# Optimization experiments

Measured on AMD Instinct MI355X. Metric: run time of the kernel, lower is better.

The kernel has to match this reference:

```python
import jax, jax.numpy as jnp
import numpy as np

WIN = 9  # window_size (isotropic, module default)
EPS = 1e-5


def _box_sum3d(x, win):
    """Sum over a win^3 box, same-size output ('same' padding). x: [B,1,D,H,W].
    The ones kernel is separable, so apply three 1D convolutions."""
    pad = win // 2
    for ax in range(3):  # spatial axes D,H,W
        kshape = [1, 1, 1, 1, 1]
        kshape[2 + ax] = win
        k = jnp.ones(kshape, x.dtype)
        padding = [(0, 0)] * 3
        padding[ax] = (pad, pad)
        x = jax.lax.conv_general_dilated(x, k, window_strides=(1, 1, 1), padding=padding)
    return x


def setup_inputs() -> dict:
    key = jax.random.key(0)
    k1, k2 = jax.random.split(key)
    shape = (2, 1, 160, 192, 160)
    y_pred = jax.random.normal(k1, shape, dtype=jnp.float32)
    y_true = jax.random.normal(k2, shape, dtype=jnp.float32)
    return {"y_pred": y_pred, "y_true": y_true}


def reference(y_pred, y_true):
    I, J = y_true, y_pred
    win_size = jnp.asarray(WIN ** 3, I.dtype)  # 729

    I_sum = _box_sum3d(I, WIN)
    J_sum = _box_sum3d(J, WIN)
    I2_sum = _box_sum3d(I * I, WIN)
    J2_sum = _box_sum3d(J * J, WIN)
    IJ_sum = _box_sum3d(I * J, WIN)

    I_mean = I_sum / win_size
    J_mean = J_sum / win_size

    cross = IJ_sum - J_mean * I_sum - I_mean * J_sum + I_mean * J_mean * win_size
    I_var = I2_sum - 2 * I_mean * I_sum + I_mean * I_mean * win_size
    J_var = J2_sum - 2 * J_mean * J_sum + J_mean * J_mean * win_size

    cc = cross * cross / (I_var * J_var + EPS)
    return -jnp.mean(cc)
```

## Files before the change

kernel.cpp:

```cpp
#include <hip/hip_runtime.h>
#include <hip/hip_fp16.h>


#define B_    2
#define D_    160
#define H_    192
#define W_    160
#define HW_   (H_*W_)

#define RS    12
#define SLS   (24*RS)
#define FS    (2*SLS)
#define RAWSZ (5*FS)
#define ZROW  (2*RAWSZ)
#define ZEND  (ZROW + 16)
#define HSUM0 ZEND
#define HCS   160
#define HRS   10
#define HSZ   (10*HCS)
#define REDU  (HSUM0 + 2*HSZ)
#define SMEM  (REDU + 8)
#define DC    80
#define ZCH   (D_/DC)
#define NMAC  ((DC+8)/2)
#define W3I   (1.0f/729.0f)
#define NTOT  9830400.0f

#if __has_builtin(__builtin_amdgcn_rcpf)
#define RCP(x) __builtin_amdgcn_rcpf(x)
#else
#define RCP(x) (1.0f/(x))
#endif

typedef _Float16 half8 __attribute__((ext_vector_type(8)));
typedef float    f32x4 __attribute__((ext_vector_type(4)));
typedef unsigned u32x2 __attribute__((ext_vector_type(2)));
#define MFMA16(a,b,c) __builtin_amdgcn_mfma_f32_16x16x32_f16((a),(b),(c),0,0,0)

#if __has_builtin(__builtin_amdgcn_permlane32_swap)
#define PL32(a,b) do { u32x2 _s = __builtin_amdgcn_permlane32_swap((a),(b),false,false); \
                       (a)=_s[0]; (b)=_s[1]; } while(0)
#else
#define PL32(a,b) asm volatile("s_nop 1\nv_permlane32_swap_b32 %0, %1" : "+v"(a), "+v"(b))
#endif
#if __has_builtin(__builtin_amdgcn_permlane16_swap)
#define PL16(a,b) do { u32x2 _s = __builtin_amdgcn_permlane16_swap((a),(b),false,false); \
                       (a)=_s[0]; (b)=_s[1]; } while(0)
#else
#define PL16(a,b) asm volatile("s_nop 1\nv_permlane16_swap_b32 %0, %1" : "+v"(a), "+v"(b))
#endif

struct __align__(8) HP { __half2 a, b; };

__global__ __launch_bounds__(256, 4) void ncc_fused(const float* __restrict__ gI,
                                                    const float* __restrict__ gJ,
                                                    float* __restrict__ out)
{
  __shared__ __align__(16) float sm[SMEM];
  const int tid  = threadIdx.x;
  const int lane = tid & 63;
  const int Q    = tid >> 6;
  const int n15  = lane & 15;
  const int q4   = lane >> 4;
  const int w0   = blockIdx.x * 16;
  const int h0   = blockIdx.y * 16;
  const int bz   = blockIdx.z;
  const int bb   = bz / ZCH;
  const int d_lo = (bz % ZCH) * DC;

  for (int i = tid; i < ZEND; i += 256) sm[i] = 0.f;

  half8 SEL;
  #pragma unroll
  for (int j = 0; j < 8; ++j) {
    const int k = 8*q4 + j;
    SEL[j] = (k >= n15 && k <= n15 + 8) ? (_Float16)1 : (_Float16)0;
  }

  bool val0 = false, val1 = false;
  int  lo0 = 0, lo1 = 0, sc0 = 0, sc1 = 0;
  const float *pi0 = gI, *pj0 = gJ, *pi1 = gI, *pj1 = gJ;
  {
    auto prep = [&](int t, bool& val, int& lo, int& sc,
                    const float*& pi, const float*& pj) {
      if (t >= 288) { val = false; return; }
      sc = t / 144;
      const int u = t - sc*144;
      const int r = u / 6, c = u - r*6;
      const int gh = h0 - 4 + r, gw = w0 - 4 + 4*c;
      val = ((unsigned)gh < (unsigned)H_) && (gw >= 0) && (gw + 3 < W_);
      lo  = sc*SLS + r*RS + 2*c;
      const long off = ((long)(bb*D_ + (d_lo - 4 + sc))*H_ + gh)*(long)W_ + gw;
      pi = gI + off; pj = gJ + off;
    };
    prep(tid, val0, lo0, sc0, pi0, pj0);
    prep((tid >= 224) ? tid + 32 : 512, val1, lo1, sc1, pi1, pj1);
  }

  int rb_[3], hb_[3];
  #pragma unroll
  for (int i = 0; i < 3; ++i) {
    int c = Q + 4*i; if (c > 9) c = 9;
    rb_[i] = (c % 5)*FS + (c / 5)*SLS;
    hb_[i] = HSUM0 + c*HCS;
  }
  const int a1r = n15*RS + 4*q4;
  const int a2r = (n15 < 8) ? ((16 + n15)*RS + 4*q4) : -1;
  const int zr  = ZROW + 4*q4;

  const int rh = tid >> 4, rw = tid & 15;
  const int rbase = HSUM0 + rw*HRS + (rh >> 1);
  const int rsh   = (rh & 1) * 16;

  float ring[5][9], S[5];
  #pragma unroll
  for (int f = 0; f < 5; ++f) {
    S[f] = 0.f;
    #pragma unroll
    for (int k = 0; k < 9; ++k) ring[f][k] = 0.f;
  }
  float acc = 0.f;

  float4 f0i = {0,0,0,0}, f0j = {0,0,0,0}, f1i = {0,0,0,0}, f1j = {0,0,0,0};
  auto fetch = [&](int sbase) {
    if (val0 && (unsigned)(sbase + sc0) < (unsigned)D_) {
      f0i = *(const float4*)pi0; f0j = *(const float4*)pj0;
    } else { f0i = make_float4(0,0,0,0); f0j = make_float4(0,0,0,0); }
    pi0 += 2*HW_; pj0 += 2*HW_;
    if (val1 && (unsigned)(sbase + sc1) < (unsigned)D_) {
      f1i = *(const float4*)pi1; f1j = *(const float4*)pj1;
    } else { f1i = make_float4(0,0,0,0); f1j = make_float4(0,0,0,0); }
    pi1 += 2*HW_; pj1 += 2*HW_;
  };

  auto stage_one = [&](int lo, float4 fi, float4 fj) {
    const __half2 i01 = __floats2half2_rn(fi.x, fi.y);
    const __half2 i23 = __floats2half2_rn(fi.z, fi.w);
    const __half2 j01 = __floats2half2_rn(fj.x, fj.y);
    const __half2 j23 = __floats2half2_rn(fj.z, fj.w);
    HP hI; hI.a = i01; hI.b = i23;
    HP hJ; hJ.a = j01; hJ.b = j23;
    HP h2; h2.a = __hmul2(i01, i01); h2.b = __hmul2(i23, i23);
    HP h3; h3.a = __hmul2(j01, j01); h3.b = __hmul2(j23, j23);
    HP h4; h4.a = __hmul2(i01, j01); h4.b = __hmul2(i23, j23);
    *(HP*)&sm[lo]        = hI;
    *(HP*)&sm[lo +   FS] = hJ;
    *(HP*)&sm[lo + 2*FS] = h2;
    *(HP*)&sm[lo + 3*FS] = h3;
    *(HP*)&sm[lo + 4*FS] = h4;
  };
  auto stage_write = [&](int buf) {
    const int b = buf * RAWSZ;
    if (val0) stage_one(b + lo0, f0i, f0j);
    if (val1) stage_one(b + lo1, f1i, f1j);
  };

  auto chain = [&](int rb, int hb) {
    const half8 A1 = *(const half8*)&sm[rb + a1r];
    const half8 A2 = (a2r >= 0) ? *(const half8*)&sm[rb + a2r]
                                : *(const half8*)&sm[zr];
    const f32x4 z = {0.f, 0.f, 0.f, 0.f};
    const f32x4 d1 = MFMA16(A1, SEL, z);
    const f32x4 d2 = MFMA16(A2, SEL, z);
    unsigned t0 = __builtin_bit_cast(unsigned, __floats2half2_rn(d1[0], d1[1]));
    unsigned t1 = __builtin_bit_cast(unsigned, __floats2half2_rn(d1[2], d1[3]));
    unsigned u0 = __builtin_bit_cast(unsigned, __floats2half2_rn(d2[0], d2[1]));
    unsigned u1 = __builtin_bit_cast(unsigned, __floats2half2_rn(d2[2], d2[3]));
    PL32(t0, u0);
    PL32(t1, u1);
    PL16(t0, u0);
    PL16(t1, u1);
    union { unsigned u[4]; half8 h; } Bv;
    Bv.u[0] = t0; Bv.u[1] = t1; Bv.u[2] = u0; Bv.u[3] = u1;
    const f32x4 dh = MFMA16(SEL, Bv.h, z);
    HP ph; ph.a = __floats2half2_rn(dh[0], dh[1]); ph.b = __floats2half2_rn(dh[2], dh[3]);
    *(HP*)&sm[hb + n15*HRS + 2*q4] = ph;
  };

  auto h2ext = [&](int addr) -> float {
    const unsigned u = *(const unsigned*)&sm[addr];
    return __half2float(__ushort_as_half((unsigned short)(u >> rsh)));
  };
  auto ring_cc = [&](int m, int hB) {
    float nA[5], nB[5];
    #pragma unroll
    for (int f = 0; f < 5; ++f) {
      nA[f] = h2ext(rbase + hB + f*HCS);
      nB[f] = h2ext(rbase + hB + (5 + f)*HCS);
    }
    float SA[5], SB[5];
    #pragma unroll
    for (int f = 0; f < 5; ++f) {
      SA[f] = S[f]  + nA[f] - ring[f][8];
      SB[f] = SA[f] + nB[f] - ring[f][7];
      S[f]  = SB[f];
      #pragma unroll
      for (int k = 8; k >= 2; --k) ring[f][k] = ring[f][k-2];
      ring[f][1] = nA[f]; ring[f][0] = nB[f];
    }
    if (m >= 4) {
      {
        const float cr = SA[4] - SA[0]*SA[1]*W3I;
        const float vi = SA[2] - SA[0]*SA[0]*W3I;
        const float vj = SA[3] - SA[1]*SA[1]*W3I;
        acc += cr*cr * RCP(vi*vj + 1e-5f);
      }
      {
        const float cr = SB[4] - SB[0]*SB[1]*W3I;
        const float vi = SB[2] - SB[0]*SB[0]*W3I;
        const float vj = SB[3] - SB[1]*SB[1]*W3I;
        acc += cr*cr * RCP(vi*vj + 1e-5f);
      }
    }
  };

  fetch(d_lo - 4);
  __syncthreads();
  stage_write(0);
  fetch(d_lo - 2);
  __syncthreads();

  for (int m = 0; m < NMAC; ++m) {
    const int rB = (m & 1) * RAWSZ;
    const int hB = (m & 1) * HSZ;
    chain(rB + rb_[0], hB + hb_[0]);
    chain(rB + rb_[1], hB + hb_[1]);
    if (Q < 2) chain(rB + rb_[2], hB + hb_[2]);
    if (m + 1 < NMAC) { stage_write((m + 1) & 1); fetch(d_lo + 2*m); }
    __syncthreads();
    ring_cc(m, hB);
  }

  float v = acc;
  #pragma unroll
  for (int off = 32; off > 0; off >>= 1)
    v += __shfl_down(v, off, 64);
  if (lane == 0) sm[REDU + Q] = v;
  __syncthreads();
  if (tid == 0) {
    const float t = sm[REDU] + sm[REDU+1] + sm[REDU+2] + sm[REDU+3];
    atomicAdd(out, -t / NTOT);
  }
}

extern "C" void kernel_launch(void* const* d_in, const int* in_sizes, int n_in,
                              void* d_out, int out_size, void* d_ws, size_t ws_size,
                              hipStream_t stream) {
  const float* J = (const float*)d_in[0];
  const float* I = (const float*)d_in[1];
  float* outp = (float*)d_out;
  hipMemsetAsync(d_out, 0, sizeof(float), stream);
  dim3 grid(W_/16, H_/16, B_*ZCH);
  ncc_fused<<<grid, dim3(256), 0, stream>>>(I, J, outp);
}
```

Before: 139.9 us.

## Software-pipeline global loads and ring updates with double register buffers

The main loop is unrolled by two, with two sets of register buffers (A and B) for the staged global loads. Each load is now issued a full step before its data is converted and written to shared memory. The ring/CC accumulation for the previous step is moved to overlap with the MFMA chains of the current step, while each step still has one barrier. This targets exposed global-load latency and barrier stalls, but adds 16 live float registers under a 4-waves-per-SIMD launch bound, which could cause spills.

```diff
diff --git a/kernel.cpp b/kernel.cpp
--- a/kernel.cpp
+++ b/kernel.cpp
@@ -121,17 +121,21 @@
   }
   float acc = 0.f;
 
-  float4 f0i = {0,0,0,0}, f0j = {0,0,0,0}, f1i = {0,0,0,0}, f1j = {0,0,0,0};
-  auto fetch = [&](int sbase) {
+  float4 a0i = {0,0,0,0}, a0j = {0,0,0,0}, a1i = {0,0,0,0}, a1j = {0,0,0,0};
+  float4 b0i = {0,0,0,0}, b0j = {0,0,0,0}, b1i = {0,0,0,0}, b1j = {0,0,0,0};
+  auto fetch_into = [&](int sbase, float4& g0i, float4& g0j,
+                                   float4& g1i, float4& g1j) {
     if (val0 && (unsigned)(sbase + sc0) < (unsigned)D_) {
-      f0i = *(const float4*)pi0; f0j = *(const float4*)pj0;
-    } else { f0i = make_float4(0,0,0,0); f0j = make_float4(0,0,0,0); }
+      g0i = *(const float4*)pi0; g0j = *(const float4*)pj0;
+    } else { g0i = make_float4(0,0,0,0); g0j = make_float4(0,0,0,0); }
     pi0 += 2*HW_; pj0 += 2*HW_;
     if (val1 && (unsigned)(sbase + sc1) < (unsigned)D_) {
-      f1i = *(const float4*)pi1; f1j = *(const float4*)pj1;
-    } else { f1i = make_float4(0,0,0,0); f1j = make_float4(0,0,0,0); }
+      g1i = *(const float4*)pi1; g1j = *(const float4*)pj1;
+    } else { g1i = make_float4(0,0,0,0); g1j = make_float4(0,0,0,0); }
     pi1 += 2*HW_; pj1 += 2*HW_;
   };
+  auto fetchA = [&](int sbase) { fetch_into(sbase, a0i, a0j, a1i, a1j); };
+  auto fetchB = [&](int sbase) { fetch_into(sbase, b0i, b0j, b1i, b1j); };
 
   auto stage_one = [&](int lo, float4 fi, float4 fj) {
     const __half2 i01 = __floats2half2_rn(fi.x, fi.y);
@@ -149,10 +153,15 @@
     *(HP*)&sm[lo + 3*FS] = h3;
     *(HP*)&sm[lo + 4*FS] = h4;
   };
-  auto stage_write = [&](int buf) {
+  auto stageA = [&](int buf) {
     const int b = buf * RAWSZ;
-    if (val0) stage_one(b + lo0, f0i, f0j);
-    if (val1) stage_one(b + lo1, f1i, f1j);
+    if (val0) stage_one(b + lo0, a0i, a0j);
+    if (val1) stage_one(b + lo1, a1i, a1j);
+  };
+  auto stageB = [&](int buf) {
+    const int b = buf * RAWSZ;
+    if (val0) stage_one(b + lo0, b0i, b0j);
+    if (val1) stage_one(b + lo1, b1i, b1j);
   };
 
   auto chain = [&](int rb, int hb) {
@@ -214,22 +223,30 @@
     }
   };
 
-  fetch(d_lo - 4);
+  fetchA(d_lo - 4);
   __syncthreads();
-  stage_write(0);
-  fetch(d_lo - 2);
+  stageA(0);
+  fetchB(d_lo - 2);
   __syncthreads();
 
-  for (int m = 0; m < NMAC; ++m) {
-    const int rB = (m & 1) * RAWSZ;
-    const int hB = (m & 1) * HSZ;
-    chain(rB + rb_[0], hB + hb_[0]);
-    chain(rB + rb_[1], hB + hb_[1]);
-    if (Q < 2) chain(rB + rb_[2], hB + hb_[2]);
-    if (m + 1 < NMAC) { stage_write((m + 1) & 1); fetch(d_lo + 2*m); }
+  for (int t = 0; t < NMAC/2; ++t) {
+    const int m0 = 2*t, m1 = 2*t + 1;
+    if (m0 + 2 < NMAC) fetchA(d_lo + 2*m0);
+    stageB(1);
+    if (t > 0) ring_cc(m0 - 1, HSZ);
+    chain(rb_[0], hb_[0]);
+    chain(rb_[1], hb_[1]);
+    if (Q < 2) chain(rb_[2], hb_[2]);
     __syncthreads();
-    ring_cc(m, hB);
-  }
+    if (m1 + 2 < NMAC) fetchB(d_lo + 2*m1);
+    if (m1 + 1 < NMAC) stageA(0);
+    ring_cc(m0, 0);
+    chain(RAWSZ + rb_[0], HSZ + hb_[0]);
+    chain(RAWSZ + rb_[1], HSZ + hb_[1]);
+    if (Q < 2) chain(RAWSZ + rb_[2], HSZ + hb_[2]);
+    __syncthreads();
+  }
+  ring_cc(NMAC - 1, HSZ);
 
   float v = acc;
   #pragma unroll
```

Result: slower. 193.5 us (+38.3%).
